# Performance work log

Measured on AMD Instinct MI355X. Metric: run time of the kernel, lower is better.

Reference implementation:

```python
import jax, jax.numpy as jnp
import numpy as np

TEMPERATURE = 0.07


def setup_inputs() -> dict:
    key = jax.random.key(0)
    k1, k2 = jax.random.split(key)
    B, D = 8192, 256
    embeddings = jax.random.normal(k1, (B, D), dtype=jnp.float32)
    ids = jax.random.randint(k2, (B,), 0, 1024, dtype=jnp.int64 if jax.config.jax_enable_x64 else jnp.int32)
    return {"embeddings": embeddings, "ids": ids}


def reference(embeddings, ids):
    B = embeddings.shape[0]
    # L2-normalize rows (F.normalize with p=2, dim=1)
    emb = embeddings / jnp.maximum(jnp.linalg.norm(embeddings, axis=1, keepdims=True), 1e-12)
    sim = (emb @ emb.T) / TEMPERATURE                      # [B, B]
    eye = jnp.eye(B, dtype=bool)
    sim = jnp.where(eye, -jnp.inf, sim)
    exp_sim = jnp.exp(sim)                                  # diag -> 0
    pos_mask = (ids[:, None] == ids[None, :]) & ~eye        # [B, B]
    pos_sum = jnp.sum(jnp.where(pos_mask, exp_sim, 0.0), axis=1)  # [B]
    all_sum = jnp.sum(exp_sim, axis=1)                      # [B]
    valid = pos_mask.any(axis=1)
    per_row = -jnp.log(pos_sum / all_sum)
    loss = jnp.sum(jnp.where(valid, per_row, 0.0))
    n_valid = jnp.sum(valid.astype(jnp.float32))
    return loss / jnp.maximum(n_valid, 1.0)
```

## Files before the change

### kernel.cpp

```cpp
#include <hip/hip_runtime.h>
#include <hip/hip_bf16.h>

#define B_SZ 8192
#define D_SZ 256
#define NTILES 2080
#define GRID_SIM 512
#define PRESCALE 4.539816004686735f

typedef __attribute__((ext_vector_type(4))) float f32x4;
typedef __attribute__((ext_vector_type(8))) short s16x8;

__global__ __launch_bounds__(256) void norm_kernel(const float* __restrict__ emb,
                                                   ushort* __restrict__ nbf,
                                                   float* __restrict__ sums) {
    sums[blockIdx.x * 64 + (threadIdx.x >> 2)] = 0.0f;

    const int wave = threadIdx.x >> 6, lane = threadIdx.x & 63;
    for (int g = blockIdx.x; g < B_SZ / 4; g += 256) {
        const int row = g * 4 + wave;
        const float4 v = ((const float4*)(emb + (size_t)row * D_SZ))[lane];
        float ss = v.x * v.x + v.y * v.y + v.z * v.z + v.w * v.w;
        #pragma unroll
        for (int m = 1; m < 64; m <<= 1) ss += __shfl_xor(ss, m, 64);
        float s = PRESCALE / fmaxf(sqrtf(ss), 1e-12f);
        __hip_bfloat16 b0 = __float2bfloat16(v.x * s);
        __hip_bfloat16 b1 = __float2bfloat16(v.y * s);
        __hip_bfloat16 b2 = __float2bfloat16(v.z * s);
        __hip_bfloat16 b3 = __float2bfloat16(v.w * s);
        ushort4 o;
        o.x = *(ushort*)&b0; o.y = *(ushort*)&b1; o.z = *(ushort*)&b2; o.w = *(ushort*)&b3;
        ((ushort4*)(nbf + (size_t)row * D_SZ))[lane] = o;
    }
}

__device__ __forceinline__ void decode_tile(int tb, int& i0, int& j0, bool& diag) {
    int bj = (int)((sqrtf(8.0f * tb + 1.0f) - 1.0f) * 0.5f);
    while ((bj + 1) * (bj + 2) / 2 <= tb) ++bj;
    while (bj * (bj + 1) / 2 > tb) --bj;
    const int bi = tb - bj * (bj + 1) / 2;
    i0 = bi * 128; j0 = bj * 128; diag = (bi == bj);
}

__device__ __forceinline__ void load_regs(s16x8 ra[4], s16x8 rb[4],
                                          const ushort* __restrict__ N,
                                          int i0, int j0, int k0,
                                          int wave, int r, int c8s) {
    const ushort* gA = N + (size_t)(i0 + wave * 32) * D_SZ + k0;
    const ushort* gB = N + (size_t)(j0 + wave * 32) * D_SZ + k0;
    #pragma unroll
    for (int q = 0; q < 4; ++q) {
        ra[q] = *(const s16x8*)(gA + (size_t)(q * 8 + r) * D_SZ + c8s);
        rb[q] = *(const s16x8*)(gB + (size_t)(q * 8 + r) * D_SZ + c8s);
    }
}

__device__ __forceinline__ void store_stage(const s16x8 ra[4], const s16x8 rb[4],
                                            ushort* bA, ushort* bB,
                                            int wave, int lane) {
    #pragma unroll
    for (int q = 0; q < 4; ++q) {
        *(s16x8*)&bA[(wave * 32 + q * 8) * 64 + lane * 8] = ra[q];
        *(s16x8*)&bB[(wave * 32 + q * 8) * 64 + lane * 8] = rb[q];
    }
}

__global__ __launch_bounds__(256) void sim_kernel(const ushort* __restrict__ N,
                                                  const int* __restrict__ ids,
                                                  float* __restrict__ all_sum,
                                                  float* __restrict__ pos_sum) {
    __shared__ ushort smem[4 * 128 * 64];

    const int t    = threadIdx.x;
    const int wave = t >> 6, lane = t & 63;
    const int wy   = wave >> 1, wx = wave & 1;
    const int r    = lane >> 3;
    const int c8s  = ((lane & 7) ^ r) * 8;
    const int myc  = lane & 15;

    int tb = blockIdx.x;
    int i0, j0; bool diag;
    decode_tile(tb, i0, j0, diag);

    s16x8 ra[4], rb[4];
    load_regs(ra, rb, N, i0, j0, 0, wave, r, c8s);

    while (true) {
        const int ntb = tb + GRID_SIM;
        const bool have_next = (ntb < NTILES);
        int ni0 = i0, nj0 = j0; bool ndiag = diag;
        if (have_next) decode_tile(ntb, ni0, nj0, ndiag);

        f32x4 acc[4][4];
        #pragma unroll
        for (int mi = 0; mi < 4; ++mi)
            #pragma unroll
            for (int ni = 0; ni < 4; ++ni)
                acc[mi][ni] = (f32x4){0.f, 0.f, 0.f, 0.f};

        #pragma unroll
        for (int kk = 0; kk < 4; ++kk) {
            ushort* bA = smem + (kk & 1) * 16384;
            ushort* bB = bA + 8192;
            store_stage(ra, rb, bA, bB, wave, lane);
            if (kk < 3)           load_regs(ra, rb, N, i0, j0, (kk + 1) * 64, wave, r, c8s);
            else if (have_next)   load_regs(ra, rb, N, ni0, nj0, 0, wave, r, c8s);
            __syncthreads();

            #pragma unroll
            for (int ks = 0; ks < 2; ++ks) {
                const int C = ks * 4 + (lane >> 4);
                const int slot = (C ^ (lane & 7)) * 8;
                s16x8 af[4], bf[4];
                #pragma unroll
                for (int mi = 0; mi < 4; ++mi)
                    af[mi] = *(const s16x8*)&bA[(wy * 64 + mi * 16 + (lane & 15)) * 64 + slot];
                #pragma unroll
                for (int ni = 0; ni < 4; ++ni)
                    bf[ni] = *(const s16x8*)&bB[(wx * 64 + ni * 16 + (lane & 15)) * 64 + slot];
                #pragma unroll
                for (int mi = 0; mi < 4; ++mi)
                    #pragma unroll
                    for (int ni = 0; ni < 4; ++ni)
                        acc[mi][ni] = __builtin_amdgcn_mfma_f32_16x16x32_bf16(
                            af[mi], bf[ni], acc[mi][ni], 0, 0, 0);
            }
        }

        float* rowAllPart = (float*)smem;
        float* rowPosPart = (float*)&smem[8192];

        int idc[4];
        #pragma unroll
        for (int ni = 0; ni < 4; ++ni)
            idc[ni] = ids[j0 + wx * 64 + ni * 16 + myc];

        float cAll[4] = {0.f, 0.f, 0.f, 0.f};
        float cPos[4] = {0.f, 0.f, 0.f, 0.f};

        #pragma unroll
        for (int mi = 0; mi < 4; ++mi) {
            float rAll[4] = {0.f, 0.f, 0.f, 0.f};
            float rPos[4] = {0.f, 0.f, 0.f, 0.f};
            const int rbase = wy * 64 + mi * 16 + (lane >> 4) * 4;
            const int4 idr  = *(const int4*)&ids[i0 + rbase];
            #pragma unroll
            for (int ni = 0; ni < 4; ++ni) {
                const int cloc = wx * 64 + ni * 16 + myc;
                #pragma unroll
                for (int rg = 0; rg < 4; ++rg) {
                    const int lr = rbase + rg;
                    float e = __builtin_amdgcn_exp2f(acc[mi][ni][rg]);
                    if (diag && lr == cloc) e = 0.0f;
                    rAll[rg] += e; cAll[ni] += e;
                    const int idrv = (rg == 0) ? idr.x : (rg == 1) ? idr.y
                                   : (rg == 2) ? idr.z : idr.w;
                    if (idrv == idc[ni]) { rPos[rg] += e; cPos[ni] += e; }
                }
            }
            #pragma unroll
            for (int rg = 0; rg < 4; ++rg) {
                rowAllPart[(rbase + rg) * 32 + wx * 16 + myc] = rAll[rg];
                rowPosPart[(rbase + rg) * 32 + wx * 16 + myc] = rPos[rg];
            }
        }

        if (!diag) {
            #pragma unroll
            for (int ni = 0; ni < 4; ++ni) {
                cAll[ni] += __shfl_xor(cAll[ni], 16, 64);
                cAll[ni] += __shfl_xor(cAll[ni], 32, 64);
                cPos[ni] += __shfl_xor(cPos[ni], 16, 64);
                cPos[ni] += __shfl_xor(cPos[ni], 32, 64);
            }
            if (lane < 16) {
                #pragma unroll
                for (int ni = 0; ni < 4; ++ni) {
                    const int gc = j0 + wx * 64 + ni * 16 + lane;
                    atomicAdd(&all_sum[gc], cAll[ni]);
                    if (cPos[ni] != 0.0f) atomicAdd(&pos_sum[gc], cPos[ni]);
                }
            }
        }

        __syncthreads();
        {
            const int row = t & 127;
            const float* src = (t >= 128) ? rowPosPart : rowAllPart;
            float s = 0.0f;
            #pragma unroll
            for (int k8 = 0; k8 < 8; ++k8) {
                const int chunk = (k8 + (row & 7)) & 7;
                const float4 v = *(const float4*)&src[row * 32 + chunk * 4];
                s += v.x + v.y + v.z + v.w;
            }
            float* dst = (t >= 128) ? pos_sum : all_sum;
            atomicAdd(&dst[i0 + row], s);
        }
        __syncthreads();

        if (!have_next) break;
        tb = ntb; i0 = ni0; j0 = nj0; diag = ndiag;
    }
}

__global__ __launch_bounds__(256) void loss_kernel(const float* __restrict__ all_sum,
                                                   const float* __restrict__ pos_sum,
                                                   float* __restrict__ out) {
    float loss = 0.0f, cnt = 0.0f;
    for (int i = threadIdx.x; i < B_SZ; i += 256) {
        float p = pos_sum[i], a = all_sum[i];
        if (p > 0.0f) { loss += logf(a) - logf(p); cnt += 1.0f; }
    }
    #pragma unroll
    for (int m = 1; m < 64; m <<= 1) {
        loss += __shfl_xor(loss, m, 64);
        cnt  += __shfl_xor(cnt, m, 64);
    }
    __shared__ float sl[4], sc[4];
    int wave = threadIdx.x >> 6, lane = threadIdx.x & 63;
    if (lane == 0) { sl[wave] = loss; sc[wave] = cnt; }
    __syncthreads();
    if (threadIdx.x == 0) {
        float L = sl[0] + sl[1] + sl[2] + sl[3];
        float C = sc[0] + sc[1] + sc[2] + sc[3];
        out[0] = L / fmaxf(C, 1.0f);
    }
}

extern "C" void kernel_launch(void* const* d_in, const int* in_sizes, int n_in,
                              void* d_out, int out_size, void* d_ws, size_t ws_size,
                              hipStream_t stream) {
    const float* emb = (const float*)d_in[0];
    const int*   ids = (const int*)d_in[1];
    float*       out = (float*)d_out;

    float*  all_sum = (float*)d_ws;
    float*  pos_sum = all_sum + B_SZ;
    ushort* nbf     = (ushort*)((char*)d_ws + 65536);

    norm_kernel<<<256, 256, 0, stream>>>(emb, nbf, all_sum);
    sim_kernel<<<GRID_SIM, 256, 0, stream>>>(nbf, ids, all_sum, pos_sum);
    loss_kernel<<<1, 256, 0, stream>>>(all_sum, pos_sum, out);
}
```

Measured before the change: 118.0 us.

## Use MFMA-fragment-ordered layout with per-wave 128x64 tiles and no LDS

The norm kernel now writes the normalized bf16 matrix in a layout matching MFMA fragments, so each wave loads its operands straight from global memory into registers without going through shared memory or barriers. Work is split into 128x64 upper-triangle tiles, one per wave, with a 1040-block grid instead of a persistent 512-block loop. The diagonal is handled by masking the straddling tiles, and row sums are reduced with shuffles plus atomics instead of an LDS reduction. The risks are that operand reuse now depends on L2/L1 rather than LDS, that the launch carries more atomics and loses prefetch overlap, and that the large per-wave accumulator set raises register pressure.

```diff
diff --git a/kernel.cpp b/kernel.cpp
--- a/kernel.cpp
+++ b/kernel.cpp
@@ -3,12 +3,12 @@
 
 #define B_SZ 8192
 #define D_SZ 256
-#define NTILES 2080
-#define GRID_SIM 512
+#define NT_WAVE 4160
 #define PRESCALE 4.539816004686735f
 
 typedef __attribute__((ext_vector_type(4))) float f32x4;
 typedef __attribute__((ext_vector_type(8))) short s16x8;
+
 
 __global__ __launch_bounds__(256) void norm_kernel(const float* __restrict__ emb,
                                                    ushort* __restrict__ nbf,
@@ -29,178 +29,126 @@
         __hip_bfloat16 b3 = __float2bfloat16(v.w * s);
         ushort4 o;
         o.x = *(ushort*)&b0; o.y = *(ushort*)&b1; o.z = *(ushort*)&b2; o.w = *(ushort*)&b3;
-        ((ushort4*)(nbf + (size_t)row * D_SZ))[lane] = o;
+        const int k0 = lane * 4;
+        const int f  = (row >> 4) * 8 + (k0 >> 5);
+        const int sl = (row & 15) + (((k0 >> 3) & 3) << 4);
+        *(ushort4*)(nbf + (size_t)f * 512 + sl * 8 + (k0 & 7)) = o;
     }
 }
 
-__device__ __forceinline__ void decode_tile(int tb, int& i0, int& j0, bool& diag) {
-    int bj = (int)((sqrtf(8.0f * tb + 1.0f) - 1.0f) * 0.5f);
-    while ((bj + 1) * (bj + 2) / 2 <= tb) ++bj;
-    while (bj * (bj + 1) / 2 > tb) --bj;
-    const int bi = tb - bj * (bj + 1) / 2;
-    i0 = bi * 128; j0 = bj * 128; diag = (bi == bj);
+__device__ __forceinline__ void decode_tile(int tb, int& i0, int& j0, bool& straddle) {
+    int bi = (int)((129.0f - sqrtf(16641.0f - 4.0f * (float)tb)) * 0.5f);
+    while ((bi + 1) * (129 - (bi + 1)) <= tb) ++bi;
+    while (bi * (129 - bi) > tb) --bi;
+    const int bj = 2 * bi + (tb - bi * (129 - bi));
+    i0 = bi * 128; j0 = bj * 64;
+    straddle = (bj - 2 * bi) < 2;
 }
 
-__device__ __forceinline__ void load_regs(s16x8 ra[4], s16x8 rb[4],
-                                          const ushort* __restrict__ N,
-                                          int i0, int j0, int k0,
-                                          int wave, int r, int c8s) {
-    const ushort* gA = N + (size_t)(i0 + wave * 32) * D_SZ + k0;
-    const ushort* gB = N + (size_t)(j0 + wave * 32) * D_SZ + k0;
+template <bool MASK>
+__device__ __forceinline__ void do_epilogue(const f32x4 (&acc)[8][4],
+                                            const int* __restrict__ ids,
+                                            float* __restrict__ all_sum,
+                                            float* __restrict__ pos_sum,
+                                            int i0, int j0, int hi, int myc) {
+    int idc[4];
     #pragma unroll
-    for (int q = 0; q < 4; ++q) {
-        ra[q] = *(const s16x8*)(gA + (size_t)(q * 8 + r) * D_SZ + c8s);
-        rb[q] = *(const s16x8*)(gB + (size_t)(q * 8 + r) * D_SZ + c8s);
+    for (int ni = 0; ni < 4; ++ni) idc[ni] = ids[j0 + ni * 16 + myc];
+
+    float cA[4] = {0.f, 0.f, 0.f, 0.f};
+    float cP[4] = {0.f, 0.f, 0.f, 0.f};
+
+    #pragma unroll
+    for (int mi = 0; mi < 8; ++mi) {
+        const int rbase = i0 + mi * 16 + hi * 4;
+        const int4 idr = *(const int4*)&ids[rbase];
+        float rA[4] = {0.f, 0.f, 0.f, 0.f};
+        float rP[4] = {0.f, 0.f, 0.f, 0.f};
+        #pragma unroll
+        for (int ni = 0; ni < 4; ++ni) {
+            const int gj = j0 + ni * 16 + myc;
+            #pragma unroll
+            for (int rg = 0; rg < 4; ++rg) {
+                float e = __builtin_amdgcn_exp2f(acc[mi][ni][rg]);
+                if (MASK) { if (gj <= rbase + rg) e = 0.0f; }
+                const int idrv = (rg == 0) ? idr.x : (rg == 1) ? idr.y
+                               : (rg == 2) ? idr.z : idr.w;
+                rA[rg] += e; cA[ni] += e;
+                if (idrv == idc[ni]) { rP[rg] += e; cP[ni] += e; }
+            }
+        }
+        #pragma unroll
+        for (int rg = 0; rg < 4; ++rg) {
+            #pragma unroll
+            for (int m = 1; m < 16; m <<= 1) {
+                rA[rg] += __shfl_xor(rA[rg], m, 64);
+                rP[rg] += __shfl_xor(rP[rg], m, 64);
+            }
+        }
+        if (myc == 0) {
+            #pragma unroll
+            for (int rg = 0; rg < 4; ++rg) {
+                atomicAdd(&all_sum[rbase + rg], rA[rg]);
+                if (rP[rg] != 0.0f) atomicAdd(&pos_sum[rbase + rg], rP[rg]);
+            }
+        }
+    }
+
+    #pragma unroll
+    for (int ni = 0; ni < 4; ++ni) {
+        cA[ni] += __shfl_xor(cA[ni], 16, 64);
+        cA[ni] += __shfl_xor(cA[ni], 32, 64);
+        cP[ni] += __shfl_xor(cP[ni], 16, 64);
+        cP[ni] += __shfl_xor(cP[ni], 32, 64);
+    }
+    if (hi == 0) {
+        #pragma unroll
+        for (int ni = 0; ni < 4; ++ni) {
+            atomicAdd(&all_sum[j0 + ni * 16 + myc], cA[ni]);
+            if (cP[ni] != 0.0f) atomicAdd(&pos_sum[j0 + ni * 16 + myc], cP[ni]);
+        }
     }
 }
 
-__device__ __forceinline__ void store_stage(const s16x8 ra[4], const s16x8 rb[4],
-                                            ushort* bA, ushort* bB,
-                                            int wave, int lane) {
+__global__ __launch_bounds__(256, 2) void sim_kernel(const ushort* __restrict__ N,
+                                                     const int* __restrict__ ids,
+                                                     float* __restrict__ all_sum,
+                                                     float* __restrict__ pos_sum) {
+    const int wave = threadIdx.x >> 6, lane = threadIdx.x & 63;
+    const int hi = lane >> 4, myc = lane & 15;
+
+    const int tb = blockIdx.x * 4 + wave;
+    int i0, j0; bool straddle;
+    decode_tile(tb, i0, j0, straddle);
+
+    f32x4 acc[8][4];
     #pragma unroll
-    for (int q = 0; q < 4; ++q) {
-        *(s16x8*)&bA[(wave * 32 + q * 8) * 64 + lane * 8] = ra[q];
-        *(s16x8*)&bB[(wave * 32 + q * 8) * 64 + lane * 8] = rb[q];
-    }
-}
+    for (int mi = 0; mi < 8; ++mi)
+        #pragma unroll
+        for (int ni = 0; ni < 4; ++ni)
+            acc[mi][ni] = (f32x4){0.f, 0.f, 0.f, 0.f};
 
-__global__ __launch_bounds__(256) void sim_kernel(const ushort* __restrict__ N,
-                                                  const int* __restrict__ ids,
-                                                  float* __restrict__ all_sum,
-                                                  float* __restrict__ pos_sum) {
-    __shared__ ushort smem[4 * 128 * 64];
+    const ushort* Ap = N + (size_t)((i0 >> 4) * 8) * 512 + (size_t)lane * 8;
+    const ushort* Bp = N + (size_t)((j0 >> 4) * 8) * 512 + (size_t)lane * 8;
 
-    const int t    = threadIdx.x;
-    const int wave = t >> 6, lane = t & 63;
-    const int wy   = wave >> 1, wx = wave & 1;
-    const int r    = lane >> 3;
-    const int c8s  = ((lane & 7) ^ r) * 8;
-    const int myc  = lane & 15;
-
-    int tb = blockIdx.x;
-    int i0, j0; bool diag;
-    decode_tile(tb, i0, j0, diag);
-
-    s16x8 ra[4], rb[4];
-    load_regs(ra, rb, N, i0, j0, 0, wave, r, c8s);
-
-    while (true) {
-        const int ntb = tb + GRID_SIM;
-        const bool have_next = (ntb < NTILES);
-        int ni0 = i0, nj0 = j0; bool ndiag = diag;
-        if (have_next) decode_tile(ntb, ni0, nj0, ndiag);
-
-        f32x4 acc[4][4];
+    #pragma unroll 1
+    for (int kc = 0; kc < 8; ++kc) {
+        s16x8 bfr[4];
         #pragma unroll
-        for (int mi = 0; mi < 4; ++mi)
+        for (int ni = 0; ni < 4; ++ni)
+            bfr[ni] = *(const s16x8*)(Bp + (size_t)(ni * 8 + kc) * 512);
+        #pragma unroll
+        for (int mi = 0; mi < 8; ++mi) {
+            const s16x8 afr = *(const s16x8*)(Ap + (size_t)(mi * 8 + kc) * 512);
             #pragma unroll
             for (int ni = 0; ni < 4; ++ni)
-                acc[mi][ni] = (f32x4){0.f, 0.f, 0.f, 0.f};
+                acc[mi][ni] = __builtin_amdgcn_mfma_f32_16x16x32_bf16(
+                    afr, bfr[ni], acc[mi][ni], 0, 0, 0);
+        }
+    }
 
-        #pragma unroll
-        for (int kk = 0; kk < 4; ++kk) {
-            ushort* bA = smem + (kk & 1) * 16384;
-            ushort* bB = bA + 8192;
-            store_stage(ra, rb, bA, bB, wave, lane);
-            if (kk < 3)           load_regs(ra, rb, N, i0, j0, (kk + 1) * 64, wave, r, c8s);
-            else if (have_next)   load_regs(ra, rb, N, ni0, nj0, 0, wave, r, c8s);
-            __syncthreads();
-
-            #pragma unroll
-            for (int ks = 0; ks < 2; ++ks) {
-                const int C = ks * 4 + (lane >> 4);
-                const int slot = (C ^ (lane & 7)) * 8;
-                s16x8 af[4], bf[4];
-                #pragma unroll
-                for (int mi = 0; mi < 4; ++mi)
-                    af[mi] = *(const s16x8*)&bA[(wy * 64 + mi * 16 + (lane & 15)) * 64 + slot];
-                #pragma unroll
-                for (int ni = 0; ni < 4; ++ni)
-                    bf[ni] = *(const s16x8*)&bB[(wx * 64 + ni * 16 + (lane & 15)) * 64 + slot];
-                #pragma unroll
-                for (int mi = 0; mi < 4; ++mi)
-                    #pragma unroll
-                    for (int ni = 0; ni < 4; ++ni)
-                        acc[mi][ni] = __builtin_amdgcn_mfma_f32_16x16x32_bf16(
-                            af[mi], bf[ni], acc[mi][ni], 0, 0, 0);
-            }
-        }
-
-        float* rowAllPart = (float*)smem;
-        float* rowPosPart = (float*)&smem[8192];
-
-        int idc[4];
-        #pragma unroll
-        for (int ni = 0; ni < 4; ++ni)
-            idc[ni] = ids[j0 + wx * 64 + ni * 16 + myc];
-
-        float cAll[4] = {0.f, 0.f, 0.f, 0.f};
-        float cPos[4] = {0.f, 0.f, 0.f, 0.f};
-
-        #pragma unroll
-        for (int mi = 0; mi < 4; ++mi) {
-            float rAll[4] = {0.f, 0.f, 0.f, 0.f};
-            float rPos[4] = {0.f, 0.f, 0.f, 0.f};
-            const int rbase = wy * 64 + mi * 16 + (lane >> 4) * 4;
-            const int4 idr  = *(const int4*)&ids[i0 + rbase];
-            #pragma unroll
-            for (int ni = 0; ni < 4; ++ni) {
-                const int cloc = wx * 64 + ni * 16 + myc;
-                #pragma unroll
-                for (int rg = 0; rg < 4; ++rg) {
-                    const int lr = rbase + rg;
-                    float e = __builtin_amdgcn_exp2f(acc[mi][ni][rg]);
-                    if (diag && lr == cloc) e = 0.0f;
-                    rAll[rg] += e; cAll[ni] += e;
-                    const int idrv = (rg == 0) ? idr.x : (rg == 1) ? idr.y
-                                   : (rg == 2) ? idr.z : idr.w;
-                    if (idrv == idc[ni]) { rPos[rg] += e; cPos[ni] += e; }
-                }
-            }
-            #pragma unroll
-            for (int rg = 0; rg < 4; ++rg) {
-                rowAllPart[(rbase + rg) * 32 + wx * 16 + myc] = rAll[rg];
-                rowPosPart[(rbase + rg) * 32 + wx * 16 + myc] = rPos[rg];
-            }
-        }
-
-        if (!diag) {
-            #pragma unroll
-            for (int ni = 0; ni < 4; ++ni) {
-                cAll[ni] += __shfl_xor(cAll[ni], 16, 64);
-                cAll[ni] += __shfl_xor(cAll[ni], 32, 64);
-                cPos[ni] += __shfl_xor(cPos[ni], 16, 64);
-                cPos[ni] += __shfl_xor(cPos[ni], 32, 64);
-            }
-            if (lane < 16) {
-                #pragma unroll
-                for (int ni = 0; ni < 4; ++ni) {
-                    const int gc = j0 + wx * 64 + ni * 16 + lane;
-                    atomicAdd(&all_sum[gc], cAll[ni]);
-                    if (cPos[ni] != 0.0f) atomicAdd(&pos_sum[gc], cPos[ni]);
-                }
-            }
-        }
-
-        __syncthreads();
-        {
-            const int row = t & 127;
-            const float* src = (t >= 128) ? rowPosPart : rowAllPart;
-            float s = 0.0f;
-            #pragma unroll
-            for (int k8 = 0; k8 < 8; ++k8) {
-                const int chunk = (k8 + (row & 7)) & 7;
-                const float4 v = *(const float4*)&src[row * 32 + chunk * 4];
-                s += v.x + v.y + v.z + v.w;
-            }
-            float* dst = (t >= 128) ? pos_sum : all_sum;
-            atomicAdd(&dst[i0 + row], s);
-        }
-        __syncthreads();
-
-        if (!have_next) break;
-        tb = ntb; i0 = ni0; j0 = nj0; diag = ndiag;
-    }
+    if (straddle) do_epilogue<true >(acc, ids, all_sum, pos_sum, i0, j0, hi, myc);
+    else          do_epilogue<false>(acc, ids, all_sum, pos_sum, i0, j0, hi, myc);
 }
 
 __global__ __launch_bounds__(256) void loss_kernel(const float* __restrict__ all_sum,
@@ -239,6 +187,6 @@
     ushort* nbf     = (ushort*)((char*)d_ws + 65536);
 
     norm_kernel<<<256, 256, 0, stream>>>(emb, nbf, all_sum);
-    sim_kernel<<<GRID_SIM, 256, 0, stream>>>(nbf, ids, all_sum, pos_sum);
+    sim_kernel<<<NT_WAVE / 4, 256, 0, stream>>>(nbf, ids, all_sum, pos_sum);
     loss_kernel<<<1, 256, 0, stream>>>(all_sum, pos_sum, out);
 }
```

Result: slower. 152.1 us (+28.9%).

## Stream operand tiles directly global-to-LDS with double-buffered async loads

Applied to the files above, without the earlier changes.

Replaces the register-staged global load plus LDS store with global_load_lds direct-to-LDS transfers, issued into the alternate buffer right after each barrier. This removes VGPR staging and the explicit ds_write instructions, which lowers register pressure. The reduction scratch moves to the upper LDS half so the next tile's prefetch into buffer 0 can overlap the epilogue. The trade-off is a full vmcnt(0) wait before every barrier, which limits how much load latency can be hidden.

```diff
diff --git a/kernel.cpp b/kernel.cpp
--- a/kernel.cpp
+++ b/kernel.cpp
@@ -41,26 +41,24 @@
     i0 = bi * 128; j0 = bj * 128; diag = (bi == bj);
 }
 
-__device__ __forceinline__ void load_regs(s16x8 ra[4], s16x8 rb[4],
-                                          const ushort* __restrict__ N,
-                                          int i0, int j0, int k0,
-                                          int wave, int r, int c8s) {
+__device__ __forceinline__ void gload16(const ushort* g, ushort* l) {
+    __builtin_amdgcn_global_load_lds(
+        (const __attribute__((address_space(1))) unsigned int*)g,
+        (__attribute__((address_space(3))) unsigned int*)l,
+        16, 0, 0);
+}
+
+__device__ __forceinline__ void issue_stage(ushort* bA,
+                                            const ushort* __restrict__ N,
+                                            int i0, int j0, int k0,
+                                            int wave, int r, int c8s) {
+    ushort* bB = bA + 8192;
     const ushort* gA = N + (size_t)(i0 + wave * 32) * D_SZ + k0;
     const ushort* gB = N + (size_t)(j0 + wave * 32) * D_SZ + k0;
     #pragma unroll
     for (int q = 0; q < 4; ++q) {
-        ra[q] = *(const s16x8*)(gA + (size_t)(q * 8 + r) * D_SZ + c8s);
-        rb[q] = *(const s16x8*)(gB + (size_t)(q * 8 + r) * D_SZ + c8s);
-    }
-}
-
-__device__ __forceinline__ void store_stage(const s16x8 ra[4], const s16x8 rb[4],
-                                            ushort* bA, ushort* bB,
-                                            int wave, int lane) {
-    #pragma unroll
-    for (int q = 0; q < 4; ++q) {
-        *(s16x8*)&bA[(wave * 32 + q * 8) * 64 + lane * 8] = ra[q];
-        *(s16x8*)&bB[(wave * 32 + q * 8) * 64 + lane * 8] = rb[q];
+        gload16(gA + (size_t)(q * 8 + r) * D_SZ + c8s, bA + (wave * 32 + q * 8) * 64);
+        gload16(gB + (size_t)(q * 8 + r) * D_SZ + c8s, bB + (wave * 32 + q * 8) * 64);
     }
 }
 
@@ -81,8 +79,7 @@
     int i0, j0; bool diag;
     decode_tile(tb, i0, j0, diag);
 
-    s16x8 ra[4], rb[4];
-    load_regs(ra, rb, N, i0, j0, 0, wave, r, c8s);
+    issue_stage(smem, N, i0, j0, 0, wave, r, c8s);
 
     while (true) {
         const int ntb = tb + GRID_SIM;
@@ -100,11 +97,13 @@
         #pragma unroll
         for (int kk = 0; kk < 4; ++kk) {
             ushort* bA = smem + (kk & 1) * 16384;
+            ushort* bW = smem + ((kk + 1) & 1) * 16384;
             ushort* bB = bA + 8192;
-            store_stage(ra, rb, bA, bB, wave, lane);
-            if (kk < 3)           load_regs(ra, rb, N, i0, j0, (kk + 1) * 64, wave, r, c8s);
-            else if (have_next)   load_regs(ra, rb, N, ni0, nj0, 0, wave, r, c8s);
+
+            asm volatile("s_waitcnt vmcnt(0)" ::: "memory");
             __syncthreads();
+            if (kk < 3)           issue_stage(bW, N, i0, j0, (kk + 1) * 64, wave, r, c8s);
+            else if (have_next)   issue_stage(bW, N, ni0, nj0, 0, wave, r, c8s);
 
             #pragma unroll
             for (int ks = 0; ks < 2; ++ks) {
@@ -126,8 +125,9 @@
             }
         }
 
-        float* rowAllPart = (float*)smem;
-        float* rowPosPart = (float*)&smem[8192];
+        __syncthreads();
+        float* rowAllPart = (float*)&smem[16384];
+        float* rowPosPart = (float*)&smem[24576];
 
         int idc[4];
         #pragma unroll
@@ -196,7 +196,6 @@
             float* dst = (t >= 128) ? pos_sum : all_sum;
             atomicAdd(&dst[i0 + row], s);
         }
-        __syncthreads();
 
         if (!have_next) break;
         tb = ntb; i0 = ni0; j0 = nj0; diag = ndiag;
```

After: 118.2 us. Within noise of the previous version (+0.2%).
